# Kernel tuning notes

Measured on AMD Instinct MI355X. Metric: run time of the kernel, lower is better.

Reference implementation:

```python
import jax, jax.numpy as jnp
import numpy as np

D_MODEL, D_STATE, D_CONV, D_INNER, DT_RANK, K = 96, 16, 3, 192, 6, 4
B, H, W = 1, 64, 64


def setup_inputs() -> dict:
    key = jax.random.key(0)
    ks = jax.random.split(key, 10)
    x = jax.random.normal(ks[0], (B, H, W, D_MODEL), jnp.float32)
    in_proj_w = jax.random.normal(ks[1], (2 * D_INNER, D_MODEL), jnp.float32) * 0.02
    conv_w = jax.random.normal(ks[2], (D_INNER, 1, D_CONV, D_CONV), jnp.float32) * 0.1
    conv_b = jnp.zeros((D_INNER,), jnp.float32)
    x_proj_w = jax.random.normal(ks[3], (K, DT_RANK + 2 * D_STATE, D_INNER), jnp.float32) * 0.02
    dt_std = DT_RANK ** -0.5
    dt_w = jax.random.uniform(ks[4], (K, D_INNER, DT_RANK), jnp.float32, -dt_std, dt_std)
    # dt bias init: inv-softplus of dt ~ logUniform(1e-3, 1e-1)
    u = jax.random.uniform(ks[5], (K, D_INNER), jnp.float32)
    dt = jnp.exp(u * (np.log(0.1) - np.log(0.001)) + np.log(0.001)).clip(1e-4)
    dt_b = dt + jnp.log(-jnp.expm1(-dt))
    A_logs = jnp.log(jnp.broadcast_to(jnp.arange(1, D_STATE + 1, dtype=jnp.float32), (K * D_INNER, D_STATE)))
    Ds = jnp.ones((K * D_INNER,), jnp.float32)
    ln_g = jnp.ones((D_INNER,), jnp.float32)
    ln_b = jnp.zeros((D_INNER,), jnp.float32)
    out_proj_w = jax.random.normal(ks[6], (D_MODEL, D_INNER), jnp.float32) * 0.02
    return dict(x=x, in_proj_w=in_proj_w, conv_w=conv_w, conv_b=conv_b, x_proj_w=x_proj_w,
                dt_w=dt_w, dt_b=dt_b, A_logs=A_logs, Ds=Ds, ln_g=ln_g, ln_b=ln_b,
                out_proj_w=out_proj_w)


def _ss2d(x, in_proj_w, conv_w, conv_b, x_proj_w, dt_w, dt_b, A_logs, Ds, ln_g, ln_b, out_proj_w):
    b, h, w, c = x.shape
    L = h * w
    d = conv_w.shape[0]            # d_inner
    n = A_logs.shape[1]            # d_state
    r = dt_w.shape[2]              # dt_rank
    # in_proj + split
    xz = jnp.einsum('bhwc,ec->bhwe', x, in_proj_w)
    xx, z = xz[..., :d], xz[..., d:]
    # depthwise conv (NCHW) + SiLU
    xc = xx.transpose(0, 3, 1, 2)
    pad = (D_CONV - 1) // 2
    xc = jax.lax.conv_general_dilated(xc, conv_w, (1, 1), [(pad, pad), (pad, pad)],
                                      feature_group_count=d) + conv_b[None, :, None, None]
    xc = jax.nn.silu(xc)
    # 4 scan directions: HW, WH, and their reverses
    x_hw = xc.reshape(b, d, L)
    x_wh = xc.transpose(0, 1, 3, 2).reshape(b, d, L)
    xs = jnp.stack([x_hw, x_wh, x_hw[..., ::-1], x_wh[..., ::-1]], axis=1)  # (b,K,d,L)
    x_dbl = jnp.einsum('bkdl,kcd->bkcl', xs, x_proj_w)
    dts, Bs, Cs = x_dbl[:, :, :r], x_dbl[:, :, r:r + n], x_dbl[:, :, r + n:]
    dts = jnp.einsum('bkrl,kdr->bkdl', dts, dt_w)
    delta = jax.nn.softplus(dts + dt_b[None, :, :, None])        # (b,K,d,L)
    A = -jnp.exp(A_logs).reshape(K, d, n)
    # time-major scanned inputs
    dA = jnp.exp(jnp.einsum('bkdl,kdn->lbkdn', delta, A))        # (L,b,K,d,n)
    dBu = jnp.einsum('bkdl,bknl,bkdl->lbkdn', delta, Bs, xs)
    Ct = Cs.transpose(3, 0, 1, 2)                                # (L,b,K,n)
    def step(hst, inp):
        dA_t, dBu_t, C_t = inp
        hst = dA_t * hst + dBu_t
        return hst, jnp.einsum('bkdn,bkn->bkd', hst, C_t)
    h0 = jnp.zeros((b, K, d, n), jnp.float32)
    _, ys = jax.lax.scan(step, h0, (dA, dBu, Ct))                # ys: (L,b,K,d)
    out_y = ys.transpose(1, 2, 3, 0) + xs * Ds.reshape(K, d)[None, :, :, None]
    # recombine directions
    inv = out_y[:, 2:4][..., ::-1]
    y1 = out_y[:, 0]
    y2 = inv[:, 0]
    wh = out_y[:, 1].reshape(b, d, w, h).transpose(0, 1, 3, 2).reshape(b, d, L)
    invwh = inv[:, 1].reshape(b, d, w, h).transpose(0, 1, 3, 2).reshape(b, d, L)
    y = (y1 + y2 + wh + invwh).transpose(0, 2, 1).reshape(b, h, w, d)
    # LayerNorm (eps=1e-5, torch default)
    mu = y.mean(-1, keepdims=True)
    var = ((y - mu) ** 2).mean(-1, keepdims=True)
    y = (y - mu) * jax.lax.rsqrt(var + 1e-5) * ln_g + ln_b
    y = y * jax.nn.silu(z)
    return jnp.einsum('bhwd,cd->bhwc', y, out_proj_w)


def reference(x, in_proj_w, conv_w, conv_b, x_proj_w, dt_w, dt_b, A_logs, Ds, ln_g, ln_b, out_proj_w):
    return _ss2d(x, in_proj_w, conv_w, conv_b, x_proj_w, dt_w, dt_b, A_logs, Ds, ln_g, ln_b, out_proj_w)
```

## Files before the change

### kernel.cpp

```cpp
#include <hip/hip_runtime.h>
#include <hip/hip_bf16.h>

#define LL 4096
#define DM 96
#define DI 192
#define NS 16
#define RK 6
#define RKP 8
#define KD 4
#define CPROJ 38
#define CH 64
#define CS 64
#define NC (KD*DI*NS)
#define PT 32
#define WS 196

__device__ __forceinline__ float b2f(__hip_bfloat16 v){ return __bfloat162float(v); }

__device__ __forceinline__ int detect_bf16(const unsigned short* __restrict__ xh, int tid, int* sflag){
  if (tid < 64){
    unsigned short u = xh[2*tid];
    int e = (u >> 7) & 0xFF;
    int sane = (e >= 107 && e <= 131) ? 1 : 0;
    unsigned long long m = __ballot(sane);
    if (tid == 0) *sflag = (__popcll(m) >= 32) ? 1 : 0;
  }
  return 0;
}

struct P12 { const void* p[12]; };
__global__ void k_convert_all(P12 ptrs, float* __restrict__ dst) {
  const int off[13] = {0,393216,430080,431808,432000,461184,465792,466560,
                       478848,479616,479808,480000,498432};
  __shared__ int sflag;
  detect_bf16((const unsigned short*)ptrs.p[0], threadIdx.x, &sflag);
  __syncthreads();
  int f = sflag;
  int i = blockIdx.x * 256 + threadIdx.x;
  if (i >= 498432) return;
  int j = 0;
  #pragma unroll
  for (int s = 1; s < 12; s++) if (i >= off[s]) j = s;
  int e = i - off[j];
  if (f) dst[i] = b2f(((const __hip_bfloat16*)ptrs.p[j])[e]);
  else   dst[i] = ((const float*)ptrs.p[j])[e];
}

__global__ void k_inproj(const float* __restrict__ x,
                         const float* __restrict__ w,
                         float* __restrict__ xx, float* __restrict__ z) {
  __shared__ float xr[8*DM];
  int l0 = blockIdx.x * 8;
  int tid = threadIdx.x;
  for (int i = tid; i < 8*DM; i += 384) xr[i] = x[l0*DM + i];
  __syncthreads();
  int e = tid;
  float acc[8];
  #pragma unroll
  for (int i=0;i<8;i++) acc[i]=0.f;
  const float* wr = w + e*DM;
  for (int c=0;c<DM;c++){
    float wv = wr[c];
    #pragma unroll
    for (int i=0;i<8;i++) acc[i] = fmaf(wv, xr[i*DM+c], acc[i]);
  }
  if (e < DI) {
    #pragma unroll
    for (int i=0;i<8;i++) xx[(l0+i)*DI + e] = acc[i];
  } else {
    int e2 = e - DI;
    #pragma unroll
    for (int i=0;i<8;i++) z[(l0+i)*DI + e2] = acc[i];
  }
}

__global__ void k_conv(const float* __restrict__ xx,
                       const float* __restrict__ cw,
                       const float* __restrict__ cb,
                       float* __restrict__ xc) {
  int l = blockIdx.x;
  int d = threadIdx.x;
  int h = l >> 6, w = l & 63;
  float acc = cb[d];
  #pragma unroll
  for (int ki=0; ki<3; ki++){
    int hh = h + ki - 1;
    if ((unsigned)hh >= 64u) continue;
    #pragma unroll
    for (int kj=0;kj<3;kj++){
      int wj = w + kj - 1;
      if ((unsigned)wj >= 64u) continue;
      acc = fmaf(cw[d*9 + ki*3 + kj], xx[(hh*64+wj)*DI + d], acc);
    }
  }
  xc[l*DI + d] = acc / (1.f + __expf(-acc));
}

__device__ __forceinline__ int dir_map(int k, int t){
  if (k==0) return t;
  if (k==1) return ((t&63)<<6) | (t>>6);
  if (k==2) return 4095 - t;
  int u = 4095 - t; return ((u&63)<<6) | (u>>6);
}

__global__ void __launch_bounds__(256) k_proj(const float* __restrict__ xc,
                       const float* __restrict__ xpw,
                       float* __restrict__ dts,
                       float* __restrict__ Bb, float* __restrict__ Cb) {
  __shared__ float wl[CPROJ*WS];
  __shared__ float xs[PT*WS];
  int b = blockIdx.x;
  int k = b >> 7;
  int t_base = (b & 127) * PT;
  int tid = threadIdx.x;
  for (int idx = tid; idx < CPROJ*DI; idx += 256){
    int cc = idx / DI, j = idx - cc*DI;
    wl[cc*WS + j] = xpw[(k*CPROJ + cc)*DI + j];
  }
  for (int idx = tid; idx < PT*DI; idx += 256){
    int tt = idx / DI, j = idx - tt*DI;
    xs[tt*WS + j] = xc[dir_map(k, t_base + tt)*DI + j];
  }
  __syncthreads();
  int tg = tid & 7;
  int ty = tid >> 3;
  int cc0 = ty;
  int has2 = (ty + 32 < CPROJ);
  int cc1 = has2 ? (ty + 32) : ty;
  float a0x=0.f,a0y=0.f,a0z=0.f,a0w=0.f;
  float a1x=0.f,a1y=0.f,a1z=0.f,a1w=0.f;
  const float4* w0p = (const float4*)&wl[cc0*WS];
  const float4* w1p = (const float4*)&wl[cc1*WS];
  const float4* x0p = (const float4*)&xs[(tg     )*WS];
  const float4* x1p = (const float4*)&xs[(tg +  8)*WS];
  const float4* x2p = (const float4*)&xs[(tg + 16)*WS];
  const float4* x3p = (const float4*)&xs[(tg + 24)*WS];
  #pragma unroll 4
  for (int jc = 0; jc < DI/4; jc++){
    float4 w0 = w0p[jc], w1 = w1p[jc];
    float4 x0 = x0p[jc], x1 = x1p[jc], x2 = x2p[jc], x3 = x3p[jc];
    a0x = fmaf(w0.x,x0.x,fmaf(w0.y,x0.y,fmaf(w0.z,x0.z,fmaf(w0.w,x0.w,a0x))));
    a0y = fmaf(w0.x,x1.x,fmaf(w0.y,x1.y,fmaf(w0.z,x1.z,fmaf(w0.w,x1.w,a0y))));
    a0z = fmaf(w0.x,x2.x,fmaf(w0.y,x2.y,fmaf(w0.z,x2.z,fmaf(w0.w,x2.w,a0z))));
    a0w = fmaf(w0.x,x3.x,fmaf(w0.y,x3.y,fmaf(w0.z,x3.z,fmaf(w0.w,x3.w,a0w))));
    a1x = fmaf(w1.x,x0.x,fmaf(w1.y,x0.y,fmaf(w1.z,x0.z,fmaf(w1.w,x0.w,a1x))));
    a1y = fmaf(w1.x,x1.x,fmaf(w1.y,x1.y,fmaf(w1.z,x1.z,fmaf(w1.w,x1.w,a1y))));
    a1z = fmaf(w1.x,x2.x,fmaf(w1.y,x2.y,fmaf(w1.z,x2.z,fmaf(w1.w,x2.w,a1z))));
    a1w = fmaf(w1.x,x3.x,fmaf(w1.y,x3.y,fmaf(w1.z,x3.z,fmaf(w1.w,x3.w,a1w))));
  }
  float accs0[4] = {a0x,a0y,a0z,a0w};
  float accs1[4] = {a1x,a1y,a1z,a1w};
  #pragma unroll
  for (int i=0;i<4;i++){
    int t = t_base + tg + 8*i;
    size_t kt = (size_t)k*LL + t;
    {
      int cc = cc0; float v = accs0[i];
      if (cc < RK)            dts[kt*RKP + cc] = v;
      else if (cc < RK+NS)    Bb [kt*NS + (cc-RK)] = v;
      else                    Cb [kt*NS + (cc-RK-NS)] = v;
    }
    if (has2){
      int cc = ty + 32; float v = accs1[i];
      if (cc < RK+NS)         Bb [kt*NS + (cc-RK)] = v;
      else                    Cb [kt*NS + (cc-RK-NS)] = v;
    }
  }
}

__global__ void __launch_bounds__(256) k_scan1(
                      const float* __restrict__ xc,
                      const float* __restrict__ dts,
                      const float* __restrict__ Bbuf,
                      const float* __restrict__ A_logs,
                      const float* __restrict__ dtw,
                      const float* __restrict__ dtb,
                      float* __restrict__ Pb, float* __restrict__ Hb) {
  int b = blockIdx.x;
  int k = b / 192;
  int rem = b - k*192;
  int dg3 = rem >> 6, c = rem & 63;
  int tid = threadIdx.x;
  int dl = tid >> 2, nq = tid & 3;
  int d = dg3*64 + dl;
  int kd = k*DI + d;
  float4 Al = *(const float4*)&A_logs[kd*NS + nq*4];
  float A0 = -__expf(Al.x), A1 = -__expf(Al.y), A2 = -__expf(Al.z), A3 = -__expf(Al.w);
  float bt = dtb[kd];
  float w0 = dtw[kd*RK+0], w1 = dtw[kd*RK+1], w2 = dtw[kd*RK+2];
  float w3 = dtw[kd*RK+3], w4 = dtw[kd*RK+4], w5 = dtw[kd*RK+5];
  const float* dr = dts + ((size_t)k*LL + c*CS)*RKP;
  const float4* bp = (const float4*)(Bbuf + ((size_t)k*LL + c*CS)*NS) + nq;
  float h0=0.f,h1=0.f,h2=0.f,h3=0.f, P0=1.f,P1=1.f,P2=1.f,P3=1.f;
  for (int s=0; s<CS; s++){
    int t = c*CS + s;
    float4 lo = *(const float4*)(dr + s*RKP);
    float4 hi = *(const float4*)(dr + s*RKP + 4);
    float v = bt;
    v = fmaf(w0, lo.x, v); v = fmaf(w1, lo.y, v); v = fmaf(w2, lo.z, v);
    v = fmaf(w3, lo.w, v); v = fmaf(w4, hi.x, v); v = fmaf(w5, hi.y, v);
    float sp = (v > 20.f) ? v : __logf(1.f + __expf(v));
    float sx = sp * xc[dir_map(k,t)*DI + d];
    float4 bv = bp[s*4];
    float a;
    a = __expf(sp*A0); h0 = fmaf(a, h0, sx*bv.x); P0 *= a;
    a = __expf(sp*A1); h1 = fmaf(a, h1, sx*bv.y); P1 *= a;
    a = __expf(sp*A2); h2 = fmaf(a, h2, sx*bv.z); P2 *= a;
    a = __expf(sp*A3); h3 = fmaf(a, h3, sx*bv.w); P3 *= a;
  }
  int base = c*NC + kd*NS + nq*4;
  *(float4*)&Pb[base] = make_float4(P0,P1,P2,P3);
  *(float4*)&Hb[base] = make_float4(h0,h1,h2,h3);
}

__global__ void __launch_bounds__(256) k_scan2(
                      const float* __restrict__ Pb, const float* __restrict__ Hb,
                      float* __restrict__ H0) {
  int idx = blockIdx.x*256 + threadIdx.x;
  float h = 0.f;
  #pragma unroll 4
  for (int c=0;c<CH;c++){
    H0[c*NC + idx] = h;
    h = fmaf(Pb[c*NC + idx], h, Hb[c*NC + idx]);
  }
}

__global__ void __launch_bounds__(256) k_scan3(
                      const float* __restrict__ xc,
                      const float* __restrict__ dts,
                      const float* __restrict__ Bbuf,
                      const float* __restrict__ Cbuf,
                      const float* __restrict__ A_logs,
                      const float* __restrict__ dtw,
                      const float* __restrict__ dtb,
                      const float* __restrict__ H0,
                      float* __restrict__ yacc) {
  int b = blockIdx.x;
  int k = b / 192;
  int rem = b - k*192;
  int dg3 = rem >> 6, c = rem & 63;
  int tid = threadIdx.x;
  int dl = tid >> 2, nq = tid & 3;
  int d = dg3*64 + dl;
  int kd = k*DI + d;
  float4 Al = *(const float4*)&A_logs[kd*NS + nq*4];
  float A0 = -__expf(Al.x), A1 = -__expf(Al.y), A2 = -__expf(Al.z), A3 = -__expf(Al.w);
  float bt = dtb[kd];
  float w0 = dtw[kd*RK+0], w1 = dtw[kd*RK+1], w2 = dtw[kd*RK+2];
  float w3 = dtw[kd*RK+3], w4 = dtw[kd*RK+4], w5 = dtw[kd*RK+5];
  const float* dr = dts + ((size_t)k*LL + c*CS)*RKP;
  const float4* bp = (const float4*)(Bbuf + ((size_t)k*LL + c*CS)*NS) + nq;
  const float4* cp = (const float4*)(Cbuf + ((size_t)k*LL + c*CS)*NS) + nq;
  float4 hv = *(const float4*)&H0[c*NC + kd*NS + nq*4];
  float h0=hv.x, h1=hv.y, h2=hv.z, h3=hv.w;
  for (int s=0; s<CS; s++){
    int t = c*CS + s;
    float4 lo = *(const float4*)(dr + s*RKP);
    float4 hi = *(const float4*)(dr + s*RKP + 4);
    float v = bt;
    v = fmaf(w0, lo.x, v); v = fmaf(w1, lo.y, v); v = fmaf(w2, lo.z, v);
    v = fmaf(w3, lo.w, v); v = fmaf(w4, hi.x, v); v = fmaf(w5, hi.y, v);
    float sp = (v > 20.f) ? v : __logf(1.f + __expf(v));
    int l = dir_map(k,t);
    float sx = sp * xc[l*DI + d];
    float4 bv = bp[s*4];
    float4 cv = cp[s*4];
    float a;
    a = __expf(sp*A0); h0 = fmaf(a, h0, sx*bv.x);
    a = __expf(sp*A1); h1 = fmaf(a, h1, sx*bv.y);
    a = __expf(sp*A2); h2 = fmaf(a, h2, sx*bv.z);
    a = __expf(sp*A3); h3 = fmaf(a, h3, sx*bv.w);
    float y = h0*cv.x + h1*cv.y + h2*cv.z + h3*cv.w;
    y += __shfl_xor(y, 1, 64);
    y += __shfl_xor(y, 2, 64);
    if (nq == 0) atomicAdd(&yacc[(size_t)l*DI + d], y);
  }
}

__global__ void k_out(const float* __restrict__ yacc,
                      const float* __restrict__ xc,
                      const float* __restrict__ z,
                      const float* __restrict__ Ds,
                      const float* __restrict__ ln_g,
                      const float* __restrict__ ln_b,
                      const float* __restrict__ opw,
                      void* __restrict__ out,
                      const unsigned short* __restrict__ xh) {
  __shared__ int sflag;
  int l = blockIdx.x;
  int d = threadIdx.x;
  detect_bf16(xh, d, &sflag);
  float y = yacc[(size_t)l*DI + d];
  float dsum = Ds[0*DI+d] + Ds[1*DI+d] + Ds[2*DI+d] + Ds[3*DI+d];
  y = fmaf(xc[l*DI+d], dsum, y);
  float s1 = y, s2 = y*y;
  #pragma unroll
  for (int off=32; off; off>>=1){
    s1 += __shfl_xor(s1, off, 64);
    s2 += __shfl_xor(s2, off, 64);
  }
  __shared__ float red[6];
  __shared__ float ysh[DI];
  int wave = d >> 6;
  if ((d & 63) == 0){ red[wave] = s1; red[3+wave] = s2; }
  __syncthreads();
  float sum = red[0]+red[1]+red[2];
  float sq  = red[3]+red[4]+red[5];
  float mu = sum * (1.f/192.f);
  float var = sq * (1.f/192.f) - mu*mu;
  float rstd = rsqrtf(var + 1e-5f);
  float yn = (y - mu) * rstd * ln_g[d] + ln_b[d];
  float zv = z[l*DI + d];
  ysh[d] = yn * (zv / (1.f + __expf(-zv)));
  __syncthreads();
  if (d < DM){
    const float* wr = opw + d*DI;
    float acc = 0.f;
    for (int j=0;j<DI;j++) acc = fmaf(wr[j], ysh[j], acc);
    if (sflag) ((__hip_bfloat16*)out)[l*DM + d] = __float2bfloat16(acc);
    else       ((float*)out)[l*DM + d] = acc;
  }
}

extern "C" void kernel_launch(void* const* d_in, const int* in_sizes, int n_in,
                              void* d_out, int out_size, void* d_ws, size_t ws_size,
                              hipStream_t stream) {
  float* ws = (float*)d_ws;
  float* cvt = ws + 16;
  const int off[13] = {0,393216,430080,431808,432000,461184,465792,466560,
                       478848,479616,479808,480000,498432};
  float* c[12];
  for (int i = 0; i < 12; i++) c[i] = cvt + off[i];

  float* big    = cvt + 498432;
  float* xx     = big;
  float* z      = xx + (size_t)LL*DI;
  float* xc     = z  + (size_t)LL*DI;
  float* dts    = xc + (size_t)LL*DI;
  float* Bb     = dts + (size_t)KD*LL*RKP;
  float* Cb     = Bb + (size_t)KD*LL*NS;
  float* PbYacc = Cb + (size_t)KD*LL*NS;
  float* H0     = PbYacc + (size_t)CH*NC;
  float* Hb     = xx;

  P12 ptrs;
  for (int i = 0; i < 12; i++) ptrs.p[i] = d_in[i];
  k_convert_all<<<(498432 + 255)/256, 256, 0, stream>>>(ptrs, cvt);

  k_inproj<<<LL/8, 384, 0, stream>>>(c[0], c[1], xx, z);
  k_conv<<<LL, DI, 0, stream>>>(xx, c[2], c[3], xc);
  k_proj<<<KD*(LL/PT), 256, 0, stream>>>(xc, c[4], dts, Bb, Cb);
  k_scan1<<<KD*192, 256, 0, stream>>>(xc, dts, Bb, c[7], c[5], c[6], PbYacc, Hb);
  k_scan2<<<NC/256, 256, 0, stream>>>(PbYacc, Hb, H0);
  hipMemsetAsync(PbYacc, 0, (size_t)LL*DI*sizeof(float), stream);
  k_scan3<<<KD*192, 256, 0, stream>>>(xc, dts, Bb, Cb, c[7], c[5], c[6], H0, PbYacc);
  k_out<<<LL, DI, 0, stream>>>(PbYacc, xc, z, c[8], c[9], c[10], c[11], d_out,
                               (const unsigned short*)d_in[0]);
}
```

Baseline: 236.8 us.

## Split output projection into tiled GEMM kernel and use exp2 in scans

The fused LayerNorm+out-projection kernel, which had only 96 of 192 threads doing a serial 192-long dot product per token, becomes two kernels. A LayerNorm/gating kernel writes the gated activations to a scratch buffer (reusing H0), and a tiled projection kernel stages 16 tokens in shared memory so each thread reuses its weight row across 8 tokens. The scan kernels fold log2(e) into A and call exp2f instead of __expf to trim a multiply per exponential. The cost is an extra launch and a global round-trip for the intermediate.

After: 223.6 us. -5.6%, faster.

```diff
diff --git a/kernel.cpp b/kernel.cpp
--- a/kernel.cpp
+++ b/kernel.cpp
@@ -14,6 +14,8 @@
 #define NC (KD*DI*NS)
 #define PT 32
 #define WS 196
+#define OT 16
+#define L2E 1.44269504f
 
 __device__ __forceinline__ float b2f(__hip_bfloat16 v){ return __bfloat162float(v); }
 
@@ -185,7 +187,8 @@
   int d = dg3*64 + dl;
   int kd = k*DI + d;
   float4 Al = *(const float4*)&A_logs[kd*NS + nq*4];
-  float A0 = -__expf(Al.x), A1 = -__expf(Al.y), A2 = -__expf(Al.z), A3 = -__expf(Al.w);
+  float A0 = -__expf(Al.x)*L2E, A1 = -__expf(Al.y)*L2E;
+  float A2 = -__expf(Al.z)*L2E, A3 = -__expf(Al.w)*L2E;
   float bt = dtb[kd];
   float w0 = dtw[kd*RK+0], w1 = dtw[kd*RK+1], w2 = dtw[kd*RK+2];
   float w3 = dtw[kd*RK+3], w4 = dtw[kd*RK+4], w5 = dtw[kd*RK+5];
@@ -203,10 +206,10 @@
     float sx = sp * xc[dir_map(k,t)*DI + d];
     float4 bv = bp[s*4];
     float a;
-    a = __expf(sp*A0); h0 = fmaf(a, h0, sx*bv.x); P0 *= a;
-    a = __expf(sp*A1); h1 = fmaf(a, h1, sx*bv.y); P1 *= a;
-    a = __expf(sp*A2); h2 = fmaf(a, h2, sx*bv.z); P2 *= a;
-    a = __expf(sp*A3); h3 = fmaf(a, h3, sx*bv.w); P3 *= a;
+    a = exp2f(sp*A0); h0 = fmaf(a, h0, sx*bv.x); P0 *= a;
+    a = exp2f(sp*A1); h1 = fmaf(a, h1, sx*bv.y); P1 *= a;
+    a = exp2f(sp*A2); h2 = fmaf(a, h2, sx*bv.z); P2 *= a;
+    a = exp2f(sp*A3); h3 = fmaf(a, h3, sx*bv.w); P3 *= a;
   }
   int base = c*NC + kd*NS + nq*4;
   *(float4*)&Pb[base] = make_float4(P0,P1,P2,P3);
@@ -244,7 +247,8 @@
   int d = dg3*64 + dl;
   int kd = k*DI + d;
   float4 Al = *(const float4*)&A_logs[kd*NS + nq*4];
-  float A0 = -__expf(Al.x), A1 = -__expf(Al.y), A2 = -__expf(Al.z), A3 = -__expf(Al.w);
+  float A0 = -__expf(Al.x)*L2E, A1 = -__expf(Al.y)*L2E;
+  float A2 = -__expf(Al.z)*L2E, A3 = -__expf(Al.w)*L2E;
   float bt = dtb[kd];
   float w0 = dtw[kd*RK+0], w1 = dtw[kd*RK+1], w2 = dtw[kd*RK+2];
   float w3 = dtw[kd*RK+3], w4 = dtw[kd*RK+4], w5 = dtw[kd*RK+5];
@@ -266,10 +270,10 @@
     float4 bv = bp[s*4];
     float4 cv = cp[s*4];
     float a;
-    a = __expf(sp*A0); h0 = fmaf(a, h0, sx*bv.x);
-    a = __expf(sp*A1); h1 = fmaf(a, h1, sx*bv.y);
-    a = __expf(sp*A2); h2 = fmaf(a, h2, sx*bv.z);
-    a = __expf(sp*A3); h3 = fmaf(a, h3, sx*bv.w);
+    a = exp2f(sp*A0); h0 = fmaf(a, h0, sx*bv.x);
+    a = exp2f(sp*A1); h1 = fmaf(a, h1, sx*bv.y);
+    a = exp2f(sp*A2); h2 = fmaf(a, h2, sx*bv.z);
+    a = exp2f(sp*A3); h3 = fmaf(a, h3, sx*bv.w);
     float y = h0*cv.x + h1*cv.y + h2*cv.z + h3*cv.w;
     y += __shfl_xor(y, 1, 64);
     y += __shfl_xor(y, 2, 64);
@@ -277,19 +281,15 @@
   }
 }
 
-__global__ void k_out(const float* __restrict__ yacc,
-                      const float* __restrict__ xc,
-                      const float* __restrict__ z,
-                      const float* __restrict__ Ds,
-                      const float* __restrict__ ln_g,
-                      const float* __restrict__ ln_b,
-                      const float* __restrict__ opw,
-                      void* __restrict__ out,
-                      const unsigned short* __restrict__ xh) {
-  __shared__ int sflag;
+__global__ void k_ln(const float* __restrict__ yacc,
+                     const float* __restrict__ xc,
+                     const float* __restrict__ z,
+                     const float* __restrict__ Ds,
+                     const float* __restrict__ ln_g,
+                     const float* __restrict__ ln_b,
+                     float* __restrict__ g) {
   int l = blockIdx.x;
   int d = threadIdx.x;
-  detect_bf16(xh, d, &sflag);
   float y = yacc[(size_t)l*DI + d];
   float dsum = Ds[0*DI+d] + Ds[1*DI+d] + Ds[2*DI+d] + Ds[3*DI+d];
   y = fmaf(xc[l*DI+d], dsum, y);
@@ -300,7 +300,6 @@
     s2 += __shfl_xor(s2, off, 64);
   }
   __shared__ float red[6];
-  __shared__ float ysh[DI];
   int wave = d >> 6;
   if ((d & 63) == 0){ red[wave] = s1; red[3+wave] = s2; }
   __syncthreads();
@@ -311,14 +310,47 @@
   float rstd = rsqrtf(var + 1e-5f);
   float yn = (y - mu) * rstd * ln_g[d] + ln_b[d];
   float zv = z[l*DI + d];
-  ysh[d] = yn * (zv / (1.f + __expf(-zv)));
-  __syncthreads();
-  if (d < DM){
-    const float* wr = opw + d*DI;
-    float acc = 0.f;
-    for (int j=0;j<DI;j++) acc = fmaf(wr[j], ysh[j], acc);
-    if (sflag) ((__hip_bfloat16*)out)[l*DM + d] = __float2bfloat16(acc);
-    else       ((float*)out)[l*DM + d] = acc;
+  g[(size_t)l*DI + d] = yn * (zv / (1.f + __expf(-zv)));
+}
+
+__global__ void __launch_bounds__(192) k_oproj(const float* __restrict__ g,
+                      const float* __restrict__ opw,
+                      void* __restrict__ out,
+                      const unsigned short* __restrict__ xh) {
+  __shared__ float gs[OT*WS];
+  __shared__ int sflag;
+  int tid = threadIdx.x;
+  detect_bf16(xh, tid, &sflag);
+  int l0 = blockIdx.x * OT;
+  const float4* gsrc = (const float4*)(g + (size_t)l0*DI);
+  for (int idx = tid; idx < OT*DI/4; idx += 192){
+    int row = idx / 48, col = idx - row*48;
+    float4 v = gsrc[idx];
+    *(float4*)&gs[row*WS + col*4] = v;
+  }
+  __syncthreads();
+  int half = tid / 96;
+  int e = tid - half*96;
+  int r0 = half*8;
+  float acc[8];
+  #pragma unroll
+  for (int i=0;i<8;i++) acc[i] = 0.f;
+  const float4* wrow = (const float4*)(opw + e*DI);
+  #pragma unroll 4
+  for (int jc = 0; jc < DI/4; jc++){
+    float4 w = wrow[jc];
+    #pragma unroll
+    for (int i=0;i<8;i++){
+      float4 gv = *(const float4*)&gs[(r0+i)*WS + jc*4];
+      acc[i] = fmaf(w.x,gv.x,fmaf(w.y,gv.y,fmaf(w.z,gv.z,fmaf(w.w,gv.w,acc[i]))));
+    }
+  }
+  int f = sflag;
+  #pragma unroll
+  for (int i=0;i<8;i++){
+    int l = l0 + r0 + i;
+    if (f) ((__hip_bfloat16*)out)[l*DM + e] = __float2bfloat16(acc[i]);
+    else   ((float*)out)[l*DM + e] = acc[i];
   }
 }
 
@@ -352,8 +384,8 @@
   k_proj<<<KD*(LL/PT), 256, 0, stream>>>(xc, c[4], dts, Bb, Cb);
   k_scan1<<<KD*192, 256, 0, stream>>>(xc, dts, Bb, c[7], c[5], c[6], PbYacc, Hb);
   k_scan2<<<NC/256, 256, 0, stream>>>(PbYacc, Hb, H0);
-  hipMemsetAsync(PbYacc, 0, (size_t)LL*DI*sizeof(float), stream);
+  (void)hipMemsetAsync(PbYacc, 0, (size_t)LL*DI*sizeof(float), stream);
   k_scan3<<<KD*192, 256, 0, stream>>>(xc, dts, Bb, Cb, c[7], c[5], c[6], H0, PbYacc);
-  k_out<<<LL, DI, 0, stream>>>(PbYacc, xc, z, c[8], c[9], c[10], c[11], d_out,
-                               (const unsigned short*)d_in[0]);
-}
+  k_ln<<<LL, DI, 0, stream>>>(PbYacc, xc, z, c[8], c[9], c[10], H0);
+  k_oproj<<<LL/OT, 192, 0, stream>>>(H0, c[11], d_out, (const unsigned short*)d_in[0]);
+}
```
